# Optimization experiments

Measured on AMD Instinct MI355X. Metric: run time of the kernel, lower is better.

Reference implementation:

```python
import jax, jax.numpy as jnp
import numpy as np

REWARD_SCALE = 1.0
DIST_NORM = 2
LATENT_DIST_THRESHOLD = 6.0

BS, N_VIEWS, N_PART, F_DIM = 128, 4, 1024, 10


def setup_inputs() -> dict:
    key = jax.random.key(0)
    k1, k2, k3, k4 = jax.random.split(key, 4)
    achieved_goal = jax.random.normal(k1, (BS, N_VIEWS, N_PART, F_DIM), jnp.float32)
    desired_goal = jax.random.normal(k2, (BS, N_VIEWS, N_PART, F_DIM), jnp.float32)
    norm_mean = jax.random.normal(k3, (F_DIM,), jnp.float32)
    norm_std = jax.random.uniform(k4, (F_DIM,), jnp.float32, minval=0.5, maxval=1.5)
    return {"achieved_goal": achieved_goal, "desired_goal": desired_goal,
            "norm_mean": norm_mean, "norm_std": norm_std}


def _pairwise_sqdist(x, y):
    # x: [bs, n, d], y: [bs, m, d] -> [bs, n, m] squared L2 ('l2_simple')
    xx = jnp.sum(x * x, axis=-1)            # [bs, n]
    yy = jnp.sum(y * y, axis=-1)            # [bs, m]
    xy = jnp.einsum('bnd,bmd->bnm', x, y)   # [bs, n, m]
    return xx[:, :, None] + yy[:, None, :] - 2.0 * xy


def _particle_mask(particles):
    # latent_classifier is None -> obj_class_cond = ones -> mask = (1 == 0) = all False
    obj_on = particles[..., -1]
    return jnp.zeros_like(obj_on, dtype=bool)


def reference(achieved_goal, desired_goal, norm_mean, norm_std):
    # unnormalize (particle_normalizer.unnormalize modeled as affine)
    state_particles = achieved_goal * norm_std + norm_mean
    goal_particles = desired_goal * norm_std + norm_mean
    bs, n_views, n_particles, _ = state_particles.shape

    state_mask = _particle_mask(state_particles)   # [bs, nv, np] bool
    goal_mask = _particle_mask(goal_particles)

    # P_mask[b,v,i,j] = state_mask[b,v,i] | goal_mask[b,v,j]
    P_mask = jnp.logical_or(state_mask[..., :, None], goal_mask[..., None, :])

    state_vis = state_particles[..., 5:9]
    state_xy = state_particles[..., :2]
    goal_vis = goal_particles[..., 5:9]
    goal_xy = goal_particles[..., :2]

    inf = jnp.asarray(jnp.inf, state_particles.dtype)
    rewards = []
    for i in range(n_views):
        sxy = state_xy[:, i]                 # [bs, np, 2]
        gxy = goal_xy[:, i]
        gmask_i = goal_mask[:, i]            # [bs, np]
        smask_i = state_mask[:, i]

        P = _pairwise_sqdist(state_vis[:, i], goal_vis[:, i])  # [bs, np_state, np_goal]
        P = jnp.where(P_mask[:, i], inf, P)

        # goal -> state direction: min over state dim (axis 1)
        min_d1 = jnp.min(P, axis=1)                            # [bs, np_goal]
        idx1 = jnp.argmin(P, axis=1)                           # [bs, np_goal]
        d_goal = jnp.take_along_axis(sxy, idx1[..., None], axis=1)  # [bs, np_goal, 2]
        xy_dist_1 = jnp.linalg.norm(gxy - d_goal, ord=DIST_NORM, axis=-1)
        xy_dist_1 = jnp.where(min_d1 > LATENT_DIST_THRESHOLD, 1.0, xy_dist_1)
        xy_dist_1 = jnp.where(gmask_i, 0.0, xy_dist_1)
        n_obj_g = jnp.maximum(jnp.sum(~gmask_i, axis=1), 1)
        reward_g2s = -jnp.sum(xy_dist_1, axis=1) / n_obj_g

        # state -> goal direction: min over goal dim (axis 2)
        min_d2 = jnp.min(P, axis=2)
        idx2 = jnp.argmin(P, axis=2)
        d_state = jnp.take_along_axis(gxy, idx2[..., None], axis=1)
        xy_dist_2 = jnp.linalg.norm(sxy - d_state, ord=DIST_NORM, axis=-1)
        xy_dist_2 = jnp.where(min_d2 > LATENT_DIST_THRESHOLD, 1.0, xy_dist_2)
        xy_dist_2 = jnp.where(smask_i, 0.0, xy_dist_2)
        n_obj_s = jnp.maximum(jnp.sum(~smask_i, axis=1), 1)
        reward_s2g = -jnp.sum(xy_dist_2, axis=1) / n_obj_s

        rv = (reward_g2s + reward_s2g) / 2.0
        no_valid = jnp.logical_or(jnp.all(gmask_i, axis=-1), jnp.all(smask_i, axis=-1))
        rv = jnp.where(no_valid, -1.0, rv)
        rewards.append(rv)

    reward = jnp.mean(jnp.stack(rewards, axis=0), axis=0)   # [bs]
    return REWARD_SCALE * reward[:, None]                    # [bs, 1]
```

## Files before the change

kernel.cpp:

```cpp
#include <hip/hip_runtime.h>
#include <cstdint>
#include <cstddef>

#define NP  1024
#define FD  10
#define NV  4
#define BSZ 128
#define TPB 256
#define RPT 4

__device__ __forceinline__ float dir_pass(
    int tid,
    const float4* rvis2, const float* rss,
    const float4* cvis2, const float* css,
    const float* __restrict__ rxyg,
    const float* __restrict__ cxyg,
    float std0, float mean0, float std1, float mean1)
{
    float4 rv[RPT];
    float  rthr[RPT];
    float  bestd[RPT];
    int    bblk[RPT];
#pragma unroll
    for (int r = 0; r < RPT; ++r) {
        int n = tid + TPB * r;
        float4 t = rvis2[n];
        rv[r] = make_float4(-0.5f * t.x, -0.5f * t.y, -0.5f * t.z, -0.5f * t.w);
        rthr[r] = 6.0f - rss[n];
        bestd[r] = 3.0e38f;
        bblk[r]  = 0;
    }

    for (int m = 0; m < NP; m += 8) {
        float4 c0 = cvis2[m + 0];
        float4 c1 = cvis2[m + 1];
        float4 c2 = cvis2[m + 2];
        float4 c3 = cvis2[m + 3];
        float4 c4 = cvis2[m + 4];
        float4 c5 = cvis2[m + 5];
        float4 c6 = cvis2[m + 6];
        float4 c7 = cvis2[m + 7];
        float4 csA = *(const float4*)(css + m);
        float4 csB = *(const float4*)(css + m + 4);
#pragma unroll
        for (int r = 0; r < RPT; ++r) {
            float4 v = rv[r];
            float d0 = fmaf(v.x, c0.x, csA.x); d0 = fmaf(v.y, c0.y, d0); d0 = fmaf(v.z, c0.z, d0); d0 = fmaf(v.w, c0.w, d0);
            float d1 = fmaf(v.x, c1.x, csA.y); d1 = fmaf(v.y, c1.y, d1); d1 = fmaf(v.z, c1.z, d1); d1 = fmaf(v.w, c1.w, d1);
            float d2 = fmaf(v.x, c2.x, csA.z); d2 = fmaf(v.y, c2.y, d2); d2 = fmaf(v.z, c2.z, d2); d2 = fmaf(v.w, c2.w, d2);
            float d3 = fmaf(v.x, c3.x, csA.w); d3 = fmaf(v.y, c3.y, d3); d3 = fmaf(v.z, c3.z, d3); d3 = fmaf(v.w, c3.w, d3);
            float d4 = fmaf(v.x, c4.x, csB.x); d4 = fmaf(v.y, c4.y, d4); d4 = fmaf(v.z, c4.z, d4); d4 = fmaf(v.w, c4.w, d4);
            float d5 = fmaf(v.x, c5.x, csB.y); d5 = fmaf(v.y, c5.y, d5); d5 = fmaf(v.z, c5.z, d5); d5 = fmaf(v.w, c5.w, d5);
            float d6 = fmaf(v.x, c6.x, csB.z); d6 = fmaf(v.y, c6.y, d6); d6 = fmaf(v.z, c6.z, d6); d6 = fmaf(v.w, c6.w, d6);
            float d7 = fmaf(v.x, c7.x, csB.w); d7 = fmaf(v.y, c7.y, d7); d7 = fmaf(v.z, c7.z, d7); d7 = fmaf(v.w, c7.w, d7);
            float p0 = fminf(fminf(d0, d1), d2);
            float p1 = fminf(fminf(d3, d4), d5);
            float p2 = fminf(d6, d7);
            float bm = fminf(fminf(p0, p1), p2);
            bool lt = bm < bestd[r];
            bestd[r] = fminf(bestd[r], bm);
            bblk[r]  = lt ? m : bblk[r];
        }
    }

    float sum = 0.0f;
#pragma unroll
    for (int r = 0; r < RPT; ++r) {
        int n  = tid + TPB * r;
        int mb = bblk[r];
        float4 v = rv[r];
        float4 csA = *(const float4*)(css + mb);
        float4 csB = *(const float4*)(css + mb + 4);
        float d[8];
        float cs[8] = {csA.x, csA.y, csA.z, csA.w, csB.x, csB.y, csB.z, csB.w};
#pragma unroll
        for (int j = 0; j < 8; ++j) {
            float4 c = cvis2[mb + j];
            float t = fmaf(v.x, c.x, cs[j]);
            t = fmaf(v.y, c.y, t);
            t = fmaf(v.z, c.z, t);
            t = fmaf(v.w, c.w, t);
            d[j] = t;
        }
        int sel = 0;
#pragma unroll
        for (int j = 7; j >= 0; --j)
            if (d[j] == bestd[r]) sel = j;
        int idx = mb + sel;

        float gx = fmaf(cxyg[(size_t)idx * FD + 0], std0, mean0);
        float gy = fmaf(cxyg[(size_t)idx * FD + 1], std1, mean1);
        float ax = fmaf(rxyg[(size_t)n * FD + 0], std0, mean0);
        float ay = fmaf(rxyg[(size_t)n * FD + 1], std1, mean1);
        float dx = ax - gx;
        float dy = ay - gy;
        float dist = sqrtf(dx * dx + dy * dy);
        if (bestd[r] > rthr[r]) dist = 1.0f;
        sum += dist;
    }
    return sum;
}

extern "C" __global__ __launch_bounds__(TPB, 4)
void chamfer_pairs(const float* __restrict__ ag, const float* __restrict__ dg,
                   const float* __restrict__ nmean, const float* __restrict__ nstd,
                   float* __restrict__ partial )
{
    __shared__ __align__(16) float smem[10240];
    float4* svis2 = (float4*)smem;
    float4* gvis2 = (float4*)(smem + 4096);
    float*  sss   = smem + 8192;
    float*  ggg   = smem + 9216;
    float*  scsh  = smem + 8192;
    float*  redbuf= smem + 9216;

    const int tid  = threadIdx.x;
    const int pair = blockIdx.x;
    const float* A = ag + (size_t)pair * (NP * FD);
    const float* G = dg + (size_t)pair * (NP * FD);

    if (tid < FD) {
        scsh[tid]      = -2.0f * nstd[tid];
        scsh[FD + tid] = -2.0f * nmean[tid];
    }
    __syncthreads();

    for (int idx = tid; idx < NP * FD; idx += TPB) {
        int n = idx / FD;
        int f = idx - n * FD;
        if (f >= 5 && f < 9) {
            float va = fmaf(A[idx], scsh[f], scsh[FD + f]);
            float vg = fmaf(G[idx], scsh[f], scsh[FD + f]);
            ((float*)&svis2[n])[f - 5] = va;
            ((float*)&gvis2[n])[f - 5] = vg;
        }
    }
    __syncthreads();

    for (int n = tid; n < NP; n += TPB) {
        float4 v = svis2[n];
        sss[n] = 0.25f * (v.x * v.x + v.y * v.y + v.z * v.z + v.w * v.w);
        float4 w = gvis2[n];
        ggg[n] = 0.25f * (w.x * w.x + w.y * w.y + w.z * w.z + w.w * w.w);
    }
    __syncthreads();

    const float std0 = nstd[0], mean0 = nmean[0];
    const float std1 = nstd[1], mean1 = nmean[1];

    float sum = dir_pass(tid, svis2, sss, gvis2, ggg, A, G, std0, mean0, std1, mean1)
              + dir_pass(tid, gvis2, ggg, svis2, sss, G, A, std0, mean0, std1, mean1);

    for (int o = 32; o > 0; o >>= 1) sum += __shfl_down(sum, o, 64);
    __syncthreads();
    if ((tid & 63) == 0) redbuf[tid >> 6] = sum;
    __syncthreads();
    if (tid == 0) {
        float s = redbuf[0] + redbuf[1] + redbuf[2] + redbuf[3];
        partial[pair] = s * (-1.0f / 2048.0f);
    }
}

extern "C" __global__ void chamfer_final(const float* __restrict__ partial,
                                         float* __restrict__ out)
{
    int b = threadIdx.x;
    if (b < BSZ) {
        float s = partial[NV * b + 0] + partial[NV * b + 1]
                + partial[NV * b + 2] + partial[NV * b + 3];
        out[b] = s * 0.25f;
    }
}

extern "C" void kernel_launch(void* const* d_in, const int* in_sizes, int n_in,
                              void* d_out, int out_size, void* d_ws, size_t ws_size,
                              hipStream_t stream)
{
    const float* ag = (const float*)d_in[0];
    const float* dg = (const float*)d_in[1];
    const float* nm = (const float*)d_in[2];
    const float* ns = (const float*)d_in[3];
    float* partial  = (float*)d_ws;

    chamfer_pairs<<<BSZ * NV, TPB, 0, stream>>>(ag, dg, nm, ns, partial);
    chamfer_final<<<1, BSZ, 0, stream>>>(partial, (float*)d_out);
}
```

Before: 212.2 us.

## Split chamfer into staging kernel and per-direction half-row blocks

Adds a staging kernel that unnormalizes the visual features and their squared norms for every particle set into a global workspace. The pair kernel then launches four times as many blocks: each handles one direction and half of the rows, reading column data straight from global memory instead of LDS. This targets the low block count and occupancy of the old kernel, where one block per pair ran both directions. The cost is an extra kernel launch, workspace traffic, and reliance on cached global reads in the inner loop.

Result: slower. 256.3 us (+20.8%).

```diff
diff --git a/kernel.cpp b/kernel.cpp
--- a/kernel.cpp
+++ b/kernel.cpp
@@ -2,46 +2,94 @@
 #include <cstdint>
 #include <cstddef>
 
-#define NP  1024
-#define FD  10
-#define NV  4
-#define BSZ 128
-#define TPB 256
-#define RPT 4
+#define NP    1024
+#define FD    10
+#define NV    4
+#define BSZ   128
+#define NPAIR (BSZ * NV)
+#define NSET  (NPAIR * 2)
+#define TPB   256
+#define RPT   2
 
-__device__ __forceinline__ float dir_pass(
-    int tid,
-    const float4* rvis2, const float* rss,
-    const float4* cvis2, const float* css,
-    const float* __restrict__ rxyg,
-    const float* __restrict__ cxyg,
-    float std0, float mean0, float std1, float mean1)
+#define OFF_CS   16777216
+#define OFF_PART 20971520
+
+
+extern "C" __global__ __launch_bounds__(256)
+void chamfer_stage(const float* __restrict__ ag, const float* __restrict__ dg,
+                   const float* __restrict__ nmean, const float* __restrict__ nstd,
+                   float* __restrict__ vis2o, float* __restrict__ cso)
 {
+    const int s   = blockIdx.x;
+    const int tid = threadIdx.x;
+    const float* src = ((s & 1) ? ag : dg) + (size_t)(s >> 1) * (NP * FD);
+    float st[4], mn[4];
+#pragma unroll
+    for (int j = 0; j < 4; ++j) {
+        st[j] = -2.0f * nstd[5 + j];
+        mn[j] = -2.0f * nmean[5 + j];
+    }
+    float4* vout = (float4*)vis2o + (size_t)s * NP;
+    float*  cout = cso + (size_t)s * NP;
+    for (int n = tid; n < NP; n += 256) {
+        const float* p = src + (size_t)n * FD + 5;
+        float v0 = fmaf(p[0], st[0], mn[0]);
+        float v1 = fmaf(p[1], st[1], mn[1]);
+        float v2 = fmaf(p[2], st[2], mn[2]);
+        float v3 = fmaf(p[3], st[3], mn[3]);
+        vout[n] = make_float4(v0, v1, v2, v3);
+        cout[n] = 0.25f * (v0 * v0 + v1 * v1 + v2 * v2 + v3 * v3);
+    }
+}
+
+extern "C" __global__ __launch_bounds__(TPB, 8)
+void chamfer_pairs(const float* __restrict__ vis2, const float* __restrict__ cs,
+                   const float* __restrict__ ag, const float* __restrict__ dg,
+                   const float* __restrict__ nmean, const float* __restrict__ nstd,
+                   float* __restrict__ partial )
+{
+    __shared__ float redbuf[TPB / 64];
+
+    const int bid  = blockIdx.x;
+    const int pd   = bid >> 1;
+    const int half = bid & 1;
+    const int pair = pd >> 1;
+    const int d    = pd & 1;
+    const int tid  = threadIdx.x;
+
+    const float4* cvis  = (const float4*)vis2 + (size_t)pd * NP;
+    const float*  ccs   = cs + (size_t)pd * NP;
+    const float4* rvis4 = (const float4*)vis2 + (size_t)(pd ^ 1) * NP;
+    const float*  rcs   = cs + (size_t)(pd ^ 1) * NP;
+
+    const float* rxyg = ((d == 0) ? ag : dg) + (size_t)pair * (NP * FD);
+    const float* cxyg = ((d == 0) ? dg : ag) + (size_t)pair * (NP * FD);
+
     float4 rv[RPT];
     float  rthr[RPT];
     float  bestd[RPT];
     int    bblk[RPT];
 #pragma unroll
     for (int r = 0; r < RPT; ++r) {
-        int n = tid + TPB * r;
-        float4 t = rvis2[n];
+        int n = half * 512 + tid + TPB * r;
+        float4 t = rvis4[n];
         rv[r] = make_float4(-0.5f * t.x, -0.5f * t.y, -0.5f * t.z, -0.5f * t.w);
-        rthr[r] = 6.0f - rss[n];
+        rthr[r] = 6.0f - rcs[n];
         bestd[r] = 3.0e38f;
         bblk[r]  = 0;
     }
 
     for (int m = 0; m < NP; m += 8) {
-        float4 c0 = cvis2[m + 0];
-        float4 c1 = cvis2[m + 1];
-        float4 c2 = cvis2[m + 2];
-        float4 c3 = cvis2[m + 3];
-        float4 c4 = cvis2[m + 4];
-        float4 c5 = cvis2[m + 5];
-        float4 c6 = cvis2[m + 6];
-        float4 c7 = cvis2[m + 7];
-        float4 csA = *(const float4*)(css + m);
-        float4 csB = *(const float4*)(css + m + 4);
+        float4 c0 = cvis[m + 0];
+        float4 c1 = cvis[m + 1];
+        float4 c2 = cvis[m + 2];
+        float4 c3 = cvis[m + 3];
+        float4 c4 = cvis[m + 4];
+        float4 c5 = cvis[m + 5];
+        float4 c6 = cvis[m + 6];
+        float4 c7 = cvis[m + 7];
+        float4 csA = *(const float4*)(ccs + m);
+        float4 csB = *(const float4*)(ccs + m + 4);
 #pragma unroll
         for (int r = 0; r < RPT; ++r) {
             float4 v = rv[r];
@@ -63,29 +111,31 @@
         }
     }
 
+    const float std0 = nstd[0], mean0 = nmean[0];
+    const float std1 = nstd[1], mean1 = nmean[1];
     float sum = 0.0f;
 #pragma unroll
     for (int r = 0; r < RPT; ++r) {
-        int n  = tid + TPB * r;
+        int n  = half * 512 + tid + TPB * r;
         int mb = bblk[r];
         float4 v = rv[r];
-        float4 csA = *(const float4*)(css + mb);
-        float4 csB = *(const float4*)(css + mb + 4);
-        float d[8];
-        float cs[8] = {csA.x, csA.y, csA.z, csA.w, csB.x, csB.y, csB.z, csB.w};
+        float4 csA = *(const float4*)(ccs + mb);
+        float4 csB = *(const float4*)(ccs + mb + 4);
+        float cse[8] = {csA.x, csA.y, csA.z, csA.w, csB.x, csB.y, csB.z, csB.w};
+        float dd[8];
 #pragma unroll
         for (int j = 0; j < 8; ++j) {
-            float4 c = cvis2[mb + j];
-            float t = fmaf(v.x, c.x, cs[j]);
+            float4 c = cvis[mb + j];
+            float t = fmaf(v.x, c.x, cse[j]);
             t = fmaf(v.y, c.y, t);
             t = fmaf(v.z, c.z, t);
             t = fmaf(v.w, c.w, t);
-            d[j] = t;
+            dd[j] = t;
         }
         int sel = 0;
 #pragma unroll
         for (int j = 7; j >= 0; --j)
-            if (d[j] == bestd[r]) sel = j;
+            if (dd[j] == bestd[r]) sel = j;
         int idx = mb + sel;
 
         float gx = fmaf(cxyg[(size_t)idx * FD + 0], std0, mean0);
@@ -98,66 +148,13 @@
         if (bestd[r] > rthr[r]) dist = 1.0f;
         sum += dist;
     }
-    return sum;
-}
-
-extern "C" __global__ __launch_bounds__(TPB, 4)
-void chamfer_pairs(const float* __restrict__ ag, const float* __restrict__ dg,
-                   const float* __restrict__ nmean, const float* __restrict__ nstd,
-                   float* __restrict__ partial )
-{
-    __shared__ __align__(16) float smem[10240];
-    float4* svis2 = (float4*)smem;
-    float4* gvis2 = (float4*)(smem + 4096);
-    float*  sss   = smem + 8192;
-    float*  ggg   = smem + 9216;
-    float*  scsh  = smem + 8192;
-    float*  redbuf= smem + 9216;
-
-    const int tid  = threadIdx.x;
-    const int pair = blockIdx.x;
-    const float* A = ag + (size_t)pair * (NP * FD);
-    const float* G = dg + (size_t)pair * (NP * FD);
-
-    if (tid < FD) {
-        scsh[tid]      = -2.0f * nstd[tid];
-        scsh[FD + tid] = -2.0f * nmean[tid];
-    }
-    __syncthreads();
-
-    for (int idx = tid; idx < NP * FD; idx += TPB) {
-        int n = idx / FD;
-        int f = idx - n * FD;
-        if (f >= 5 && f < 9) {
-            float va = fmaf(A[idx], scsh[f], scsh[FD + f]);
-            float vg = fmaf(G[idx], scsh[f], scsh[FD + f]);
-            ((float*)&svis2[n])[f - 5] = va;
-            ((float*)&gvis2[n])[f - 5] = vg;
-        }
-    }
-    __syncthreads();
-
-    for (int n = tid; n < NP; n += TPB) {
-        float4 v = svis2[n];
-        sss[n] = 0.25f * (v.x * v.x + v.y * v.y + v.z * v.z + v.w * v.w);
-        float4 w = gvis2[n];
-        ggg[n] = 0.25f * (w.x * w.x + w.y * w.y + w.z * w.z + w.w * w.w);
-    }
-    __syncthreads();
-
-    const float std0 = nstd[0], mean0 = nmean[0];
-    const float std1 = nstd[1], mean1 = nmean[1];
-
-    float sum = dir_pass(tid, svis2, sss, gvis2, ggg, A, G, std0, mean0, std1, mean1)
-              + dir_pass(tid, gvis2, ggg, svis2, sss, G, A, std0, mean0, std1, mean1);
 
     for (int o = 32; o > 0; o >>= 1) sum += __shfl_down(sum, o, 64);
-    __syncthreads();
     if ((tid & 63) == 0) redbuf[tid >> 6] = sum;
     __syncthreads();
     if (tid == 0) {
         float s = redbuf[0] + redbuf[1] + redbuf[2] + redbuf[3];
-        partial[pair] = s * (-1.0f / 2048.0f);
+        partial[bid] = s;
     }
 }
 
@@ -166,9 +163,10 @@
 {
     int b = threadIdx.x;
     if (b < BSZ) {
-        float s = partial[NV * b + 0] + partial[NV * b + 1]
-                + partial[NV * b + 2] + partial[NV * b + 3];
-        out[b] = s * 0.25f;
+        float s = 0.0f;
+#pragma unroll
+        for (int i = 0; i < 16; ++i) s += partial[b * 16 + i];
+        out[b] = s * (-1.0f / 8192.0f);
     }
 }
 
@@ -180,8 +178,13 @@
     const float* dg = (const float*)d_in[1];
     const float* nm = (const float*)d_in[2];
     const float* ns = (const float*)d_in[3];
-    float* partial  = (float*)d_ws;
 
-    chamfer_pairs<<<BSZ * NV, TPB, 0, stream>>>(ag, dg, nm, ns, partial);
+    char*  ws      = (char*)d_ws;
+    float* vis2    = (float*)(ws);
+    float* csbuf   = (float*)(ws + OFF_CS);
+    float* partial = (float*)(ws + OFF_PART);
+
+    chamfer_stage<<<NSET, 256, 0, stream>>>(ag, dg, nm, ns, vis2, csbuf);
+    chamfer_pairs<<<NSET * 2, TPB, 0, stream>>>(vis2, csbuf, ag, dg, nm, ns, partial);
     chamfer_final<<<1, BSZ, 0, stream>>>(partial, (float*)d_out);
 }
```
